# Kernel tuning notes

Hardware: AMD Instinct MI355X
Metric: run time of the kernel (lower is better)

## Reference

```python
import jax, jax.numpy as jnp
import numpy as np

H, D, BLK, R = 12, 64, 64, 3  # heads, size_per_head, block size, rand blocks
NEG = -1e9


def setup_inputs() -> dict:
    key = jax.random.key(0)
    ks = jax.random.split(key, 6)
    B, S, W = 2, 4096, H * D
    M = S // BLK
    return {
        "from_tensor": jax.random.normal(ks[0], (B, S, W), jnp.float32),
        "to_tensor": jax.random.normal(ks[1], (B, S, W), jnp.float32),
        "Wq": jax.random.normal(ks[2], (W, H * D), jnp.float32) * 0.02,
        "bq": jnp.zeros((H * D,), jnp.float32),
        "Wk": jax.random.normal(ks[3], (W, H * D), jnp.float32) * 0.02,
        "bk": jnp.zeros((H * D,), jnp.float32),
        "Wv": jax.random.normal(ks[4], (W, H * D), jnp.float32) * 0.02,
        "bv": jnp.zeros((H * D,), jnp.float32),
        "to_mask": jnp.ones((B, S), jnp.int32),
        "rand_attn": jax.random.randint(ks[5], (H, M - 2, R), 0, M - 2, jnp.int32),
    }


def _bigbird_block_sparse(from_tensor, to_tensor, Wq, bq, Wk, bk, Wv, bv, to_mask, rand_attn):
    B, S, _ = from_tensor.shape
    M = S // BLK
    scale = 1.0 / np.sqrt(D).astype(np.float32)

    # QKV projections -> [B,H,S,D]
    q = (from_tensor @ Wq + bq).reshape(B, S, H, D).transpose(0, 2, 1, 3)
    k = (to_tensor @ Wk + bk).reshape(B, S, H, D).transpose(0, 2, 1, 3)
    v = (to_tensor @ Wv + bv).reshape(B, S, H, D).transpose(0, 2, 1, 3)

    bq_ = q.reshape(B, H, M, BLK, D)
    bk_ = k.reshape(B, H, M, BLK, D)
    bv_ = v.reshape(B, H, M, BLK, D)

    tm = to_mask.astype(q.dtype)          # [B,S]
    bm = tm.reshape(B, M, BLK)            # [B,M,BLK]

    # gather random key/value blocks per head: [B,H,M-2,R*BLK,D]
    ha = jnp.arange(H)[:, None, None]
    gk = bk_[:, ha, rand_attn].reshape(B, H, M - 2, R * BLK, D)
    gv = bv_[:, ha, rand_attn].reshape(B, H, M - 2, R * BLK, D)
    gm = bm[:, rand_attn].reshape(B, H, M - 2, R * BLK)

    def full_row(qblk):  # first/last query blocks attend to everything
        s = jnp.einsum('bhqd,bhkd->bhqk', qblk, k) * scale + (1 - tm)[:, None, None, :] * NEG
        return jnp.einsum('bhqk,bhkd->bhqd', jax.nn.softmax(s, -1), v)

    def sparse_row(qblk, k_cat, v_cat, m_cat):  # [B,H,BLK,D] x [B,H,L,D]
        s = jnp.einsum('bhqd,bhkd->bhqk', qblk, k_cat) * scale + (1 - m_cat)[:, :, None, :] * NEG
        return jnp.einsum('bhqk,bhkd->bhqd', jax.nn.softmax(s, -1), v_cat)

    c_first = full_row(bq_[:, :, 0])
    c_last = full_row(bq_[:, :, M - 1])

    # second row: blocks [0,1,2,last] + rand
    k2 = jnp.concatenate([bk_[:, :, 0], bk_[:, :, 1], bk_[:, :, 2], bk_[:, :, M - 1], gk[:, :, 0]], axis=2)
    v2 = jnp.concatenate([bv_[:, :, 0], bv_[:, :, 1], bv_[:, :, 2], bv_[:, :, M - 1], gv[:, :, 0]], axis=2)
    m2s = jnp.concatenate([bm[:, 0], bm[:, 1], bm[:, 2], bm[:, M - 1]], axis=-1)
    m2 = jnp.concatenate([jnp.broadcast_to(m2s[:, None], (B, H, 4 * BLK)), gm[:, :, 0]], axis=-1)
    c_second = sparse_row(bq_[:, :, 1], k2, v2, m2)

    # second-to-last row: blocks [0,M-3,M-2,M-1] + rand
    k3 = jnp.concatenate([bk_[:, :, 0], bk_[:, :, M - 3], bk_[:, :, M - 2], bk_[:, :, M - 1], gk[:, :, M - 3]], axis=2)
    v3 = jnp.concatenate([bv_[:, :, 0], bv_[:, :, M - 3], bv_[:, :, M - 2], bv_[:, :, M - 1], gv[:, :, M - 3]], axis=2)
    m3s = jnp.concatenate([bm[:, 0], bm[:, M - 3], bm[:, M - 2], bm[:, M - 1]], axis=-1)
    m3 = jnp.concatenate([jnp.broadcast_to(m3s[:, None], (B, H, 4 * BLK)), gm[:, :, M - 3]], axis=-1)
    c_secondlast = sparse_row(bq_[:, :, M - 2], k3, v3, m3)

    # middle rows 2..M-3: band(prev,self,next) + rand + global first/last blocks
    L = M - 4
    band_k = jnp.concatenate([bk_[:, :, 1:M - 3], bk_[:, :, 2:M - 2], bk_[:, :, 3:M - 1]], axis=3)  # [B,H,L,3BLK,D]
    band_v = jnp.concatenate([bv_[:, :, 1:M - 3], bv_[:, :, 2:M - 2], bv_[:, :, 3:M - 1]], axis=3)
    band_m = jnp.concatenate([bm[:, 1:M - 3], bm[:, 2:M - 2], bm[:, 3:M - 1]], axis=-1)  # [B,L,3BLK]

    k_mid = jnp.concatenate([
        band_k, gk[:, :, 1:M - 3],
        jnp.broadcast_to(bk_[:, :, 0:1], (B, H, L, BLK, D)),
        jnp.broadcast_to(bk_[:, :, M - 1:M], (B, H, L, BLK, D))], axis=3)
    v_mid = jnp.concatenate([
        band_v, gv[:, :, 1:M - 3],
        jnp.broadcast_to(bv_[:, :, 0:1], (B, H, L, BLK, D)),
        jnp.broadcast_to(bv_[:, :, M - 1:M], (B, H, L, BLK, D))], axis=3)
    m_mid = jnp.concatenate([
        jnp.broadcast_to(band_m[:, None], (B, H, L, 3 * BLK)),
        gm[:, :, 1:M - 3],
        jnp.broadcast_to(bm[:, None, None, 0], (B, H, L, BLK)),
        jnp.broadcast_to(bm[:, None, None, M - 1], (B, H, L, BLK))], axis=-1)

    s_mid = jnp.einsum('bhlqd,bhlkd->bhlqk', bq_[:, :, 2:M - 2], k_mid) * scale
    s_mid = s_mid + (1 - m_mid)[:, :, :, None, :] * NEG
    c_mid = jnp.einsum('bhlqk,bhlkd->bhlqd', jax.nn.softmax(s_mid, -1), v_mid)

    ctx = jnp.concatenate([
        c_first[:, :, None], c_second[:, :, None], c_mid,
        c_secondlast[:, :, None], c_last[:, :, None]], axis=2)  # [B,H,M,BLK,D]
    return ctx.reshape(B, H, S, D).transpose(0, 2, 1, 3)  # [B,S,H,D]


def reference(from_tensor, to_tensor, Wq, bq, Wk, bk, Wv, bv, to_mask, rand_attn):
    return _bigbird_block_sparse(from_tensor, to_tensor, Wq, bq, Wk, bk, Wv, bv, to_mask, rand_attn)
```

## Files before the change

kernel.cpp:

```cpp
#include <hip/hip_runtime.h>

typedef __attribute__((ext_vector_type(4))) float f32x4;
typedef __attribute__((ext_vector_type(8))) __bf16 bf16x8;
typedef __attribute__((ext_vector_type(8))) unsigned short u16x8;
typedef __attribute__((ext_vector_type(4))) unsigned short u16x4;
typedef __attribute__((ext_vector_type(2))) unsigned int u32x2;

#define LOG2E 1.4426950408889634f

__device__ __forceinline__ unsigned short f2bf(float f) {
  unsigned u = __builtin_bit_cast(unsigned, f);
  u += 0x7fffu + ((u >> 16) & 1u);
  return (unsigned short)(u >> 16);
}

__device__ __forceinline__ unsigned cvtpk(float lo, float hi) {
  unsigned r;
  asm("v_cvt_pk_bf16_f32 %0, %1, %2" : "=v"(r) : "v"(lo), "v"(hi));
  return r;
}

__device__ __forceinline__ f32x4 mfma16(bf16x8 a, bf16x8 b, f32x4 c) {
  return __builtin_amdgcn_mfma_f32_16x16x32_bf16(a, b, c, 0, 0, 0);
}

__device__ __forceinline__ void gload_lds16(const void* g, void* l) {
  __builtin_amdgcn_global_load_lds(
      (const __attribute__((address_space(1))) void*)g,
      (__attribute__((address_space(3))) void*)l, 16, 0, 0);
}

#define NQK 6291456
#define NX 6291456
#define NW 589824

__global__ __launch_bounds__(256) void prep_kernel(
    const float* __restrict__ Wq, const float* __restrict__ Wk,
    const float* __restrict__ Wv, const float* __restrict__ from_t,
    const float* __restrict__ to_t, unsigned short* __restrict__ Wt,
    unsigned short* __restrict__ xb) {
  __shared__ float tile[64][65];
  const int bid = blockIdx.x;
  const int t = threadIdx.x;
  if (bid < 432) {
    const int z = bid / 144, rest = bid % 144;
    const float* __restrict__ src = (z == 0) ? Wq : (z == 1) ? Wk : Wv;
    unsigned short* __restrict__ dst = Wt + (size_t)z * NW;
    const int k0 = (rest / 12) * 64, n0 = (rest % 12) * 64;
    const int r = t >> 4, c4 = (t & 15) * 4;
#pragma unroll
    for (int p = 0; p < 4; ++p) {
      int rr = r + p * 16;
      f32x4 v = *(const f32x4*)(src + (size_t)(k0 + rr) * 768 + n0 + c4);
#pragma unroll
      for (int j = 0; j < 4; ++j) tile[rr][c4 + j] = v[j];
    }
    __syncthreads();
#pragma unroll
    for (int p = 0; p < 4; ++p) {
      int rn = r + p * 16;
      u16x4 o;
#pragma unroll
      for (int j = 0; j < 4; ++j) o[j] = f2bf(tile[c4 + j][rn]);
      *(u16x4*)(dst + (size_t)(n0 + rn) * 768 + k0 + c4) = o;
    }
  } else {
    const int idx = bid - 432;
    const int y = idx / 3072, xi = idx % 3072;
    const float* __restrict__ src = y ? to_t : from_t;
    unsigned short* __restrict__ dst = xb + (size_t)y * NX;
    const size_t i = ((size_t)xi * 256 + t) * 8;
    f32x4 a = *(const f32x4*)(src + i);
    f32x4 b = *(const f32x4*)(src + i + 4);
    u16x8 o;
#pragma unroll
    for (int j = 0; j < 4; ++j) { o[j] = f2bf(a[j]); o[j + 4] = f2bf(b[j]); }
    *(u16x8*)(dst + i) = o;
  }
}

__global__ __launch_bounds__(256) void qkv_gemm_kernel(
    const unsigned short* __restrict__ Xb, const unsigned short* __restrict__ Wt,
    const float* __restrict__ bq, const float* __restrict__ bk,
    const float* __restrict__ bv, unsigned short* __restrict__ qkvQK,
    unsigned short* __restrict__ vt, int zoff, int cpx) {
  __shared__ unsigned short A_lds[2][8192];
  __shared__ unsigned short B_lds[2][8192];
  const int bid0 = blockIdx.x;
  const int bid = (bid0 & 7) * cpx + (bid0 >> 3);
  const int z = zoff + bid / 384;
  const int rem = bid % 384;
  const int bm = rem / 6, bn = rem % 6;
  const unsigned short* __restrict__ X = Xb + (z ? (size_t)NX : 0);
  const unsigned short* __restrict__ Wz = Wt + (size_t)z * NW;
  const float* __restrict__ bias = (z == 0) ? bq : (z == 1) ? bk : bv;
  const int t = threadIdx.x, lane = t & 63, w = t >> 6;
  const int wm = (w >> 1) * 64, wn = (w & 1) * 64;
  const int l15 = lane & 15, cc = lane >> 4;

  f32x4 acc[4][4];
#pragma unroll
  for (int i = 0; i < 4; ++i)
#pragma unroll
    for (int j = 0; j < 4; ++j) acc[i][j] = (f32x4){0.f, 0.f, 0.f, 0.f};

  const unsigned short* Abase = X + (size_t)bm * 128 * 768;
  const unsigned short* Bbase = Wz + (size_t)bn * 128 * 768;

  auto STAGE = [&](int ks, int bufi) {
#pragma unroll
    for (int p = 0; p < 4; ++p) {
      int wb = p * 4 + w;
      int ch = wb * 64 + lane;
      int r = ch >> 3, sl = ch & 7;
      int g = sl ^ (r & 7);
      gload_lds16(Abase + (size_t)r * 768 + ks * 64 + g * 8,
                  &A_lds[bufi][wb * 512]);
      gload_lds16(Bbase + (size_t)r * 768 + ks * 64 + g * 8,
                  &B_lds[bufi][wb * 512]);
    }
  };

  STAGE(0, 0);
  __syncthreads();

  for (int ks = 0; ks < 12; ++ks) {
    const int cur = ks & 1;
    if (ks < 11) STAGE(ks + 1, cur ^ 1);

    bf16x8 af[4][2], bfr[4][2];
#pragma unroll
    for (int mi = 0; mi < 4; ++mi) {
      int row = wm + mi * 16 + l15;
      const char* rp = (const char*)A_lds[cur] + row * 128;
#pragma unroll
      for (int kk = 0; kk < 2; ++kk)
        af[mi][kk] = *(const bf16x8*)(rp + (((cc + 4 * kk) ^ (row & 7)) << 4));
    }
#pragma unroll
    for (int ni = 0; ni < 4; ++ni) {
      int row = wn + ni * 16 + l15;
      const char* rp = (const char*)B_lds[cur] + row * 128;
#pragma unroll
      for (int kk = 0; kk < 2; ++kk)
        bfr[ni][kk] = *(const bf16x8*)(rp + (((cc + 4 * kk) ^ (row & 7)) << 4));
    }
#pragma unroll
    for (int kk = 0; kk < 2; ++kk)
#pragma unroll
      for (int mi = 0; mi < 4; ++mi)
#pragma unroll
        for (int ni = 0; ni < 4; ++ni)
          acc[mi][ni] = mfma16(af[mi][kk], bfr[ni][kk], acc[mi][ni]);
    __syncthreads();
  }

  if (z < 2) {
    const float qscale = (z == 0) ? 0.125f * LOG2E : 1.0f;
    unsigned short* __restrict__ dst = qkvQK + (size_t)z * NQK;
#pragma unroll
    for (int ni = 0; ni < 4; ++ni) {
      int gn = bn * 128 + wn + ni * 16 + l15;
      float bv_ = bias[gn];
      int hh = gn >> 6, dd = gn & 63;
#pragma unroll
      for (int mi = 0; mi < 4; ++mi) {
#pragma unroll
        for (int r = 0; r < 4; ++r) {
          int gm = bm * 128 + wm + mi * 16 + cc * 4 + r;
          int bb = gm >> 12, s = gm & 4095;
          float val = (acc[mi][ni][r] + bv_) * qscale;
          dst[((((size_t)bb * 12 + hh) * 4096 + s) * 64) + dd] = f2bf(val);
        }
      }
    }
  } else {
#pragma unroll
    for (int ni = 0; ni < 4; ++ni) {
      int gn = bn * 128 + wn + ni * 16 + l15;
      float bv_ = bias[gn];
      int hh = gn >> 6, dd = gn & 63;
#pragma unroll
      for (int mi = 0; mi < 4; ++mi) {
        int gm0 = bm * 128 + wm + mi * 16 + cc * 4;
        int bb = gm0 >> 12, s0 = gm0 & 4095;
        u16x4 o;
#pragma unroll
        for (int r = 0; r < 4; ++r) o[r] = f2bf(acc[mi][ni][r] + bv_);
        *(u16x4*)(vt + ((size_t)(bb * 12 + hh) * 64 + dd) * 4096 + s0) = o;
      }
    }
  }
}

__global__ __launch_bounds__(256) void attn_kernel(
    const unsigned short* __restrict__ qkvQK, const unsigned short* __restrict__ vt,
    const int* __restrict__ to_mask, const int* __restrict__ rand_attn,
    float* __restrict__ out, float* __restrict__ part_o,
    float* __restrict__ part_ml) {
  __shared__ unsigned short K_lds[2][4096];
  __shared__ unsigned short VT_lds[2][4096];
  __shared__ unsigned short P_lds[4][1024];
  __shared__ float penal[8][64];
  __shared__ int blist[8];

  const int bid0 = blockIdx.x;
  const int bid = (bid0 & 7) * 234 + (bid0 >> 3);
  const int bh = bid / 78, r78 = bid % 78;
  const int h = bh % 12, b = bh / 12;
  const int t = threadIdx.x, lane = t & 63, w = t >> 6;
  const int l15 = lane & 15, cc = lane >> 4;

  int m, nblk, chunk = 0;
  bool full;
  if (r78 < 62) {
    full = false;
    m = r78 + 1;
    nblk = (m == 1 || m == 62) ? 7 : 8;
    if (t == 0) {
      const int* rp = rand_attn + ((size_t)h * 62 + (m - 1)) * 3;
      if (m == 1) {
        blist[0] = 0; blist[1] = 1; blist[2] = 2; blist[3] = 63;
        blist[4] = rp[0]; blist[5] = rp[1]; blist[6] = rp[2];
      } else if (m == 62) {
        blist[0] = 0; blist[1] = 61; blist[2] = 62; blist[3] = 63;
        blist[4] = rp[0]; blist[5] = rp[1]; blist[6] = rp[2];
      } else {
        blist[0] = m - 1; blist[1] = m; blist[2] = m + 1;
        blist[3] = rp[0]; blist[4] = rp[1]; blist[5] = rp[2];
        blist[6] = 0; blist[7] = 63;
      }
    }
  } else {
    full = true;
    int fr = r78 - 62;
    chunk = fr & 7;
    m = (fr >> 3) ? 63 : 0;
    nblk = 8;
    if (t < 8) blist[t] = chunk * 8 + t;
  }

  const unsigned short* qp = qkvQK + (((size_t)b * 12 + h) * 4096 + m * 64) * 64;
  const unsigned short* kp = qkvQK + NQK + (((size_t)b * 12 + h) * 4096) * 64;
  const unsigned short* vtp = vt + (((size_t)b * 12 + h) * 64) * 4096;

  int loff[2];
  const unsigned short *kpl[2], *vpl[2];
#pragma unroll
  for (int p = 0; p < 2; ++p) {
    int wb = p * 4 + w;
    int ch = wb * 64 + lane;
    int rr = ch >> 3;
    int g = (ch & 7) ^ (rr & 7);
    loff[p] = wb * 512;
    kpl[p] = kp + rr * 64 + g * 8;
    vpl[p] = vtp + rr * 4096 + g * 8;
  }

  bf16x8 aq[2];
  {
    int qrow = w * 16 + l15;
    aq[0] = *(const bf16x8*)(qp + qrow * 64 + cc * 8);
    aq[1] = *(const bf16x8*)(qp + qrow * 64 + 32 + cc * 8);
  }

  float m_run = -INFINITY, l_run = 0.f;
  f32x4 o_acc[4];
#pragma unroll
  for (int dg = 0; dg < 4; ++dg) o_acc[dg] = (f32x4){0.f, 0.f, 0.f, 0.f};

  char* pw = (char*)P_lds[w];
  const int swz = (l15 & 7) << 4;

  auto STAGE = [&](int kb, int bufi) {
    const size_t ko = (size_t)kb * 4096;
    const size_t vo = (size_t)kb * 64;
    gload_lds16(kpl[0] + ko, &K_lds[bufi][loff[0]]);
    gload_lds16(kpl[1] + ko, &K_lds[bufi][loff[1]]);
    gload_lds16(vpl[0] + vo, &VT_lds[bufi][loff[0]]);
    gload_lds16(vpl[1] + vo, &VT_lds[bufi][loff[1]]);
  };

  __syncthreads();

  {
    int ib = w;
#pragma unroll
    for (int pp = 0; pp < 2; ++pp, ib += 4)
      if (ib < nblk)
        penal[ib][lane] =
            (1.0f - (float)to_mask[(size_t)b * 4096 + blist[ib] * 64 + lane]) *
            (-1e9f * LOG2E);
  }
  STAGE(blist[0], 0);
  __syncthreads();

  for (int ib = 0; ib < nblk; ++ib) {
    const int cur = ib & 1;
    if (ib + 1 < nblk) STAGE(blist[ib + 1], cur ^ 1);

    float sm[4][4];
    const char* kbase = (const char*)K_lds[cur];
    __builtin_amdgcn_s_setprio(1);
#pragma unroll
    for (int kg = 0; kg < 4; ++kg) {
      int krow = kg * 16 + l15;
      const char* rp = kbase + krow * 128;
      int sz = (krow & 7) << 4;
      bf16x8 k0 = *(const bf16x8*)(rp + ((cc << 4) ^ sz));
      bf16x8 k1 = *(const bf16x8*)(rp + (((cc + 4) << 4) ^ sz));
      f32x4 zz = (f32x4){0.f, 0.f, 0.f, 0.f};
      zz = mfma16(k0, aq[0], zz);
      zz = mfma16(k1, aq[1], zz);
      f32x4 pen = *(const f32x4*)(&penal[ib][kg * 16 + cc * 4]);
#pragma unroll
      for (int r = 0; r < 4; ++r) sm[kg][r] = zz[r] + pen[r];
    }
    __builtin_amdgcn_s_setprio(0);

    float mk[4];
#pragma unroll
    for (int kg = 0; kg < 4; ++kg)
      mk[kg] = fmaxf(fmaxf(sm[kg][0], sm[kg][1]), fmaxf(sm[kg][2], sm[kg][3]));
    float mx = fmaxf(fmaxf(mk[0], mk[1]), fmaxf(mk[2], mk[3]));
    mx = fmaxf(mx, __shfl_xor(mx, 16, 64));
    mx = fmaxf(mx, __shfl_xor(mx, 32, 64));

    if (!__all(mx - m_run <= 8.0f)) {
      float mn = fmaxf(m_run, mx);
      float fac = exp2f(m_run - mn);
      m_run = mn;
      l_run *= fac;
      float fr_[4];
#pragma unroll
      for (int r = 0; r < 4; ++r) fr_[r] = __shfl(fac, cc * 4 + r, 64);
#pragma unroll
      for (int dg = 0; dg < 4; ++dg)
#pragma unroll
        for (int r = 0; r < 4; ++r) o_acc[dg][r] *= fr_[r];
    }

    float p_[4][4];
#pragma unroll
    for (int kg = 0; kg < 4; ++kg)
#pragma unroll
      for (int r = 0; r < 4; ++r) p_[kg][r] = exp2f(sm[kg][r] - m_run);
    float ss[4];
#pragma unroll
    for (int kg = 0; kg < 4; ++kg)
      ss[kg] = (p_[kg][0] + p_[kg][1]) + (p_[kg][2] + p_[kg][3]);
    float rs = (ss[0] + ss[1]) + (ss[2] + ss[3]);
    rs += __shfl_xor(rs, 16, 64);
    rs += __shfl_xor(rs, 32, 64);
    l_run += rs;

#pragma unroll
    for (int kg = 0; kg < 4; ++kg) {
      u32x2 wv;
      wv[0] = cvtpk(p_[kg][0], p_[kg][1]);
      wv[1] = cvtpk(p_[kg][2], p_[kg][3]);
      *(u32x2*)(pw + l15 * 128 + ((kg * 32 + cc * 8) ^ swz)) = wv;
    }
    __builtin_amdgcn_wave_barrier();
    bf16x8 ap0 = *(const bf16x8*)(pw + l15 * 128 + ((cc << 4) ^ swz));
    bf16x8 ap1 = *(const bf16x8*)(pw + l15 * 128 + (((cc + 4) << 4) ^ swz));

    const char* vbase = (const char*)VT_lds[cur];
    __builtin_amdgcn_s_setprio(1);
#pragma unroll
    for (int dg = 0; dg < 4; ++dg) {
      int drow = dg * 16 + l15;
      const char* vb = vbase + drow * 128;
      int sz = (drow & 7) << 4;
      bf16x8 v0 = *(const bf16x8*)(vb + ((cc << 4) ^ sz));
      bf16x8 v1 = *(const bf16x8*)(vb + (((cc + 4) << 4) ^ sz));
      o_acc[dg] = mfma16(ap0, v0, o_acc[dg]);
      o_acc[dg] = mfma16(ap1, v1, o_acc[dg]);
    }
    __builtin_amdgcn_s_setprio(0);
    __syncthreads();
  }

  if (!full) {
    float inv[4];
#pragma unroll
    for (int r = 0; r < 4; ++r) inv[r] = 1.0f / __shfl(l_run, cc * 4 + r, 64);
#pragma unroll
    for (int r = 0; r < 4; ++r) {
      int s = m * 64 + w * 16 + cc * 4 + r;
#pragma unroll
      for (int dg = 0; dg < 4; ++dg) {
        int d = dg * 16 + l15;
        out[(((size_t)b * 4096 + s) * 12 + h) * 64 + d] = o_acc[dg][r] * inv[r];
      }
    }
  } else {
    const int row = (b * 12 + h) * 2 + (m ? 1 : 0);
    float* po = part_o + (((size_t)row * 8 + chunk) * 64) * 64;
    float* pml = part_ml + ((size_t)row * 8 + chunk) * 128;
#pragma unroll
    for (int r = 0; r < 4; ++r) {
      int q = w * 16 + cc * 4 + r;
#pragma unroll
      for (int dg = 0; dg < 4; ++dg) {
        int d = dg * 16 + l15;
        po[q * 64 + d] = o_acc[dg][r];
      }
    }
    if (cc == 0) {
      pml[w * 16 + l15] = m_run;
      pml[64 + w * 16 + l15] = l_run;
    }
  }
}

__global__ __launch_bounds__(256) void combine_kernel(
    const float* __restrict__ part_o, const float* __restrict__ part_ml,
    float* __restrict__ out) {
  const int row = blockIdx.x;
  const int b = row / 24, h = (row >> 1) % 12, m = (row & 1) ? 63 : 0;
  const int t = threadIdx.x;
  const int q = t >> 2, d0 = (t & 3) * 16;

  float mc[8], lc[8];
  float M = -INFINITY;
#pragma unroll
  for (int c = 0; c < 8; ++c) {
    const float* pml = part_ml + ((size_t)row * 8 + c) * 128;
    mc[c] = pml[q];
    lc[c] = pml[64 + q];
    M = fmaxf(M, mc[c]);
  }
  float wgt[8], L = 0.f;
#pragma unroll
  for (int c = 0; c < 8; ++c) {
    wgt[c] = exp2f(mc[c] - M);
    L += wgt[c] * lc[c];
  }
  f32x4 acc[4];
#pragma unroll
  for (int j = 0; j < 4; ++j) acc[j] = (f32x4){0.f, 0.f, 0.f, 0.f};
#pragma unroll
  for (int c = 0; c < 8; ++c) {
    const float* po = part_o + (((size_t)row * 8 + c) * 64 + q) * 64 + d0;
#pragma unroll
    for (int j = 0; j < 4; ++j) {
      f32x4 v = *(const f32x4*)(po + j * 4);
#pragma unroll
      for (int e = 0; e < 4; ++e) acc[j][e] += wgt[c] * v[e];
    }
  }
  const float inv = 1.0f / L;
  const int s = m * 64 + q;
  float* op = out + (((size_t)b * 4096 + s) * 12 + h) * 64 + d0;
#pragma unroll
  for (int j = 0; j < 4; ++j) {
    f32x4 v;
#pragma unroll
    for (int e = 0; e < 4; ++e) v[e] = acc[j][e] * inv;
    *(f32x4*)(op + j * 4) = v;
  }
}

extern "C" void kernel_launch(void* const* d_in, const int* in_sizes, int n_in,
                              void* d_out, int out_size, void* d_ws,
                              size_t ws_size, hipStream_t stream) {
  (void)in_sizes; (void)n_in; (void)out_size;
  const float* from_t = (const float*)d_in[0];
  const float* to_t = (const float*)d_in[1];
  const float* Wq = (const float*)d_in[2];
  const float* bq = (const float*)d_in[3];
  const float* Wk = (const float*)d_in[4];
  const float* bk = (const float*)d_in[5];
  const float* Wv = (const float*)d_in[6];
  const float* bv = (const float*)d_in[7];
  const int* to_mask = (const int*)d_in[8];
  const int* rand_attn = (const int*)d_in[9];
  float* out = (float*)d_out;

  unsigned short* Wt = (unsigned short*)d_ws;
  unsigned short* qkvQK = Wt + (size_t)3 * NW;
  unsigned short* Xb = qkvQK + (size_t)2 * NQK;

  const size_t part_elems = (size_t)48 * 8 * 64 * 64 + (size_t)48 * 8 * 128;
  const size_t fused_bytes =
      ((size_t)3 * NW + 2 * NQK + 2 * NX + NQK) * 2 + part_elems * 4;

  if (ws_size >= fused_bytes) {
    unsigned short* vt = Xb + (size_t)2 * NX;
    float* part_o = (float*)Xb;
    float* part_ml = part_o + (size_t)48 * 8 * 64 * 64;

    prep_kernel<<<dim3(6576), dim3(256), 0, stream>>>(Wq, Wk, Wv, from_t, to_t,
                                                      Wt, Xb);
    qkv_gemm_kernel<<<dim3(1152), dim3(256), 0, stream>>>(
        Xb, Wt, bq, bk, bv, qkvQK, vt, 0, 144);
    attn_kernel<<<dim3(1872), dim3(256), 0, stream>>>(
        qkvQK, vt, to_mask, rand_attn, out, part_o, part_ml);
    combine_kernel<<<dim3(48), dim3(256), 0, stream>>>(part_o, part_ml, out);
  } else {
    unsigned short* vt = Xb;
    float* part_o = (float*)(Xb + (size_t)NX);
    float* part_ml = part_o + (size_t)48 * 8 * 64 * 64;

    prep_kernel<<<dim3(6576), dim3(256), 0, stream>>>(Wq, Wk, Wv, from_t, to_t,
                                                      Wt, Xb);
    qkv_gemm_kernel<<<dim3(768), dim3(256), 0, stream>>>(
        Xb, Wt, bq, bk, bv, qkvQK, vt, 0, 96);
    qkv_gemm_kernel<<<dim3(384), dim3(256), 0, stream>>>(
        Xb, Wt, bq, bk, bv, qkvQK, vt, 2, 48);
    attn_kernel<<<dim3(1872), dim3(256), 0, stream>>>(
        qkvQK, vt, to_mask, rand_attn, out, part_o, part_ml);
    combine_kernel<<<dim3(48), dim3(256), 0, stream>>>(part_o, part_ml, out);
  }
}
```

Before: 115.1 us.

## Halve QKV GEMM k-tile, load V fragments directly from global in attention

The QKV GEMM now stages 32-wide k slices instead of 64, which halves its LDS footprint and doubles the number of loop iterations and barriers. The attention kernel drops the V^T LDS staging and loads V fragments straight from global memory into registers at the start of each block iteration. It also fuses the exp/sum/pack softmax loops and sets launch bounds to 4 blocks per SM. The goal is higher occupancy from less LDS use. The cost is exposed global-load latency for V and extra synchronisation in the GEMM.

After: 159.9 us. +39.0%, slower.

```diff
diff --git a/kernel.cpp b/kernel.cpp
--- a/kernel.cpp
+++ b/kernel.cpp
@@ -84,8 +84,8 @@
     const float* __restrict__ bq, const float* __restrict__ bk,
     const float* __restrict__ bv, unsigned short* __restrict__ qkvQK,
     unsigned short* __restrict__ vt, int zoff, int cpx) {
-  __shared__ unsigned short A_lds[2][8192];
-  __shared__ unsigned short B_lds[2][8192];
+  __shared__ unsigned short A_lds[2][4096];
+  __shared__ unsigned short B_lds[2][4096];
   const int bid0 = blockIdx.x;
   const int bid = (bid0 & 7) * cpx + (bid0 >> 3);
   const int z = zoff + bid / 384;
@@ -109,14 +109,14 @@
 
   auto STAGE = [&](int ks, int bufi) {
 #pragma unroll
-    for (int p = 0; p < 4; ++p) {
+    for (int p = 0; p < 2; ++p) {
       int wb = p * 4 + w;
       int ch = wb * 64 + lane;
-      int r = ch >> 3, sl = ch & 7;
-      int g = sl ^ (r & 7);
-      gload_lds16(Abase + (size_t)r * 768 + ks * 64 + g * 8,
+      int r = ch >> 2, sl = ch & 3;
+      int g = sl ^ (r & 3);
+      gload_lds16(Abase + (size_t)r * 768 + ks * 32 + g * 8,
                   &A_lds[bufi][wb * 512]);
-      gload_lds16(Bbase + (size_t)r * 768 + ks * 64 + g * 8,
+      gload_lds16(Bbase + (size_t)r * 768 + ks * 32 + g * 8,
                   &B_lds[bufi][wb * 512]);
     }
   };
@@ -124,34 +124,28 @@
   STAGE(0, 0);
   __syncthreads();
 
-  for (int ks = 0; ks < 12; ++ks) {
+  for (int ks = 0; ks < 24; ++ks) {
     const int cur = ks & 1;
-    if (ks < 11) STAGE(ks + 1, cur ^ 1);
-
-    bf16x8 af[4][2], bfr[4][2];
+    if (ks < 23) STAGE(ks + 1, cur ^ 1);
+
+    bf16x8 af[4], bfr[4];
 #pragma unroll
     for (int mi = 0; mi < 4; ++mi) {
       int row = wm + mi * 16 + l15;
-      const char* rp = (const char*)A_lds[cur] + row * 128;
-#pragma unroll
-      for (int kk = 0; kk < 2; ++kk)
-        af[mi][kk] = *(const bf16x8*)(rp + (((cc + 4 * kk) ^ (row & 7)) << 4));
+      af[mi] = *(const bf16x8*)((const char*)A_lds[cur] + row * 64 +
+                                ((cc ^ (row & 3)) << 4));
     }
 #pragma unroll
     for (int ni = 0; ni < 4; ++ni) {
       int row = wn + ni * 16 + l15;
-      const char* rp = (const char*)B_lds[cur] + row * 128;
-#pragma unroll
-      for (int kk = 0; kk < 2; ++kk)
-        bfr[ni][kk] = *(const bf16x8*)(rp + (((cc + 4 * kk) ^ (row & 7)) << 4));
-    }
-#pragma unroll
-    for (int kk = 0; kk < 2; ++kk)
-#pragma unroll
-      for (int mi = 0; mi < 4; ++mi)
-#pragma unroll
-        for (int ni = 0; ni < 4; ++ni)
-          acc[mi][ni] = mfma16(af[mi][kk], bfr[ni][kk], acc[mi][ni]);
+      bfr[ni] = *(const bf16x8*)((const char*)B_lds[cur] + row * 64 +
+                                 ((cc ^ (row & 3)) << 4));
+    }
+#pragma unroll
+    for (int mi = 0; mi < 4; ++mi)
+#pragma unroll
+      for (int ni = 0; ni < 4; ++ni)
+        acc[mi][ni] = mfma16(af[mi], bfr[ni], acc[mi][ni]);
     __syncthreads();
   }
 
@@ -193,13 +187,12 @@
   }
 }
 
-__global__ __launch_bounds__(256) void attn_kernel(
+__global__ __launch_bounds__(256, 4) void attn_kernel(
     const unsigned short* __restrict__ qkvQK, const unsigned short* __restrict__ vt,
     const int* __restrict__ to_mask, const int* __restrict__ rand_attn,
     float* __restrict__ out, float* __restrict__ part_o,
     float* __restrict__ part_ml) {
   __shared__ unsigned short K_lds[2][4096];
-  __shared__ unsigned short VT_lds[2][4096];
   __shared__ unsigned short P_lds[4][1024];
   __shared__ float penal[8][64];
   __shared__ int blist[8];
@@ -245,7 +238,7 @@
   const unsigned short* vtp = vt + (((size_t)b * 12 + h) * 64) * 4096;
 
   int loff[2];
-  const unsigned short *kpl[2], *vpl[2];
+  const unsigned short* kpl[2];
 #pragma unroll
   for (int p = 0; p < 2; ++p) {
     int wb = p * 4 + w;
@@ -254,8 +247,8 @@
     int g = (ch & 7) ^ (rr & 7);
     loff[p] = wb * 512;
     kpl[p] = kp + rr * 64 + g * 8;
-    vpl[p] = vtp + rr * 4096 + g * 8;
-  }
+  }
+  const unsigned short* vbase_ = vtp + (size_t)l15 * 4096 + cc * 8;
 
   bf16x8 aq[2];
   {
@@ -274,11 +267,8 @@
 
   auto STAGE = [&](int kb, int bufi) {
     const size_t ko = (size_t)kb * 4096;
-    const size_t vo = (size_t)kb * 64;
     gload_lds16(kpl[0] + ko, &K_lds[bufi][loff[0]]);
     gload_lds16(kpl[1] + ko, &K_lds[bufi][loff[1]]);
-    gload_lds16(vpl[0] + vo, &VT_lds[bufi][loff[0]]);
-    gload_lds16(vpl[1] + vo, &VT_lds[bufi][loff[1]]);
   };
 
   __syncthreads();
@@ -297,7 +287,16 @@
 
   for (int ib = 0; ib < nblk; ++ib) {
     const int cur = ib & 1;
+    const int kb = blist[ib];
     if (ib + 1 < nblk) STAGE(blist[ib + 1], cur ^ 1);
+
+    bf16x8 vf0[4], vf1[4];
+#pragma unroll
+    for (int dg = 0; dg < 4; ++dg) {
+      const unsigned short* cp = vbase_ + (size_t)dg * 16 * 4096 + kb * 64;
+      vf0[dg] = *(const bf16x8*)(cp);
+      vf1[dg] = *(const bf16x8*)(cp + 32);
+    }
 
     float sm[4][4];
     const char* kbase = (const char*)K_lds[cur];
@@ -340,42 +339,30 @@
         for (int r = 0; r < 4; ++r) o_acc[dg][r] *= fr_[r];
     }
 
-    float p_[4][4];
-#pragma unroll
-    for (int kg = 0; kg < 4; ++kg)
-#pragma unroll
-      for (int r = 0; r < 4; ++r) p_[kg][r] = exp2f(sm[kg][r] - m_run);
-    float ss[4];
-#pragma unroll
-    for (int kg = 0; kg < 4; ++kg)
-      ss[kg] = (p_[kg][0] + p_[kg][1]) + (p_[kg][2] + p_[kg][3]);
-    float rs = (ss[0] + ss[1]) + (ss[2] + ss[3]);
+    float rs = 0.f;
+#pragma unroll
+    for (int kg = 0; kg < 4; ++kg) {
+      float p0 = exp2f(sm[kg][0] - m_run), p1 = exp2f(sm[kg][1] - m_run);
+      float p2 = exp2f(sm[kg][2] - m_run), p3 = exp2f(sm[kg][3] - m_run);
+      rs += (p0 + p1) + (p2 + p3);
+      u32x2 wv;
+      wv[0] = cvtpk(p0, p1);
+      wv[1] = cvtpk(p2, p3);
+      *(u32x2*)(pw + l15 * 128 + ((kg * 32 + cc * 8) ^ swz)) = wv;
+    }
     rs += __shfl_xor(rs, 16, 64);
     rs += __shfl_xor(rs, 32, 64);
     l_run += rs;
 
-#pragma unroll
-    for (int kg = 0; kg < 4; ++kg) {
-      u32x2 wv;
-      wv[0] = cvtpk(p_[kg][0], p_[kg][1]);
-      wv[1] = cvtpk(p_[kg][2], p_[kg][3]);
-      *(u32x2*)(pw + l15 * 128 + ((kg * 32 + cc * 8) ^ swz)) = wv;
-    }
     __builtin_amdgcn_wave_barrier();
     bf16x8 ap0 = *(const bf16x8*)(pw + l15 * 128 + ((cc << 4) ^ swz));
     bf16x8 ap1 = *(const bf16x8*)(pw + l15 * 128 + (((cc + 4) << 4) ^ swz));
 
-    const char* vbase = (const char*)VT_lds[cur];
     __builtin_amdgcn_s_setprio(1);
 #pragma unroll
     for (int dg = 0; dg < 4; ++dg) {
-      int drow = dg * 16 + l15;
-      const char* vb = vbase + drow * 128;
-      int sz = (drow & 7) << 4;
-      bf16x8 v0 = *(const bf16x8*)(vb + ((cc << 4) ^ sz));
-      bf16x8 v1 = *(const bf16x8*)(vb + (((cc + 4) << 4) ^ sz));
-      o_acc[dg] = mfma16(ap0, v0, o_acc[dg]);
-      o_acc[dg] = mfma16(ap1, v1, o_acc[dg]);
+      o_acc[dg] = mfma16(ap0, vf0[dg], o_acc[dg]);
+      o_acc[dg] = mfma16(ap1, vf1[dg], o_acc[dg]);
     }
     __builtin_amdgcn_s_setprio(0);
     __syncthreads();
```

## Deepen attention K/V prefetch to triple-stage ring and use fine-grained vmcnt waits

Applied to the files above, without the earlier changes.

The attention kernel grows its K/V LDS ring from 2 to 4 buffers and prefetches two blocks ahead. It replaces the full __syncthreads at the end of each iteration with explicit vmcnt waits and a single barrier at the top. The QKV GEMM gets the same treatment with partial vmcnt waits, so the next stage's global-to-LDS loads can stay in flight while compute proceeds. Other changes drop the s_setprio hints and fuse the exp/sum/pack loops. The cost is twice the LDS use in attention, which may lower occupancy, and correctness now depends on hand-counted vmcnt values matching the number of issued loads.

Measured after the change: 116.7 us. About the same (+1.4%).

```diff
diff --git a/kernel.cpp b/kernel.cpp
--- a/kernel.cpp
+++ b/kernel.cpp
@@ -122,11 +122,17 @@
   };
 
   STAGE(0, 0);
-  __syncthreads();
 
   for (int ks = 0; ks < 12; ++ks) {
     const int cur = ks & 1;
-    if (ks < 11) STAGE(ks + 1, cur ^ 1);
+    if (ks < 11) {
+      STAGE(ks + 1, cur ^ 1);
+      asm volatile("s_waitcnt vmcnt(8)" ::: "memory");
+    } else {
+      asm volatile("s_waitcnt vmcnt(0)" ::: "memory");
+    }
+    __builtin_amdgcn_s_barrier();
+    __builtin_amdgcn_sched_barrier(0);
 
     bf16x8 af[4][2], bfr[4][2];
 #pragma unroll
@@ -152,7 +158,8 @@
 #pragma unroll
         for (int ni = 0; ni < 4; ++ni)
           acc[mi][ni] = mfma16(af[mi][kk], bfr[ni][kk], acc[mi][ni]);
-    __syncthreads();
+    asm volatile("s_waitcnt lgkmcnt(0)" ::: "memory");
+    __builtin_amdgcn_s_barrier();
   }
 
   if (z < 2) {
@@ -198,8 +205,8 @@
     const int* __restrict__ to_mask, const int* __restrict__ rand_attn,
     float* __restrict__ out, float* __restrict__ part_o,
     float* __restrict__ part_ml) {
-  __shared__ unsigned short K_lds[2][4096];
-  __shared__ unsigned short VT_lds[2][4096];
+  __shared__ unsigned short K_lds[4][4096];
+  __shared__ unsigned short VT_lds[4][4096];
   __shared__ unsigned short P_lds[4][1024];
   __shared__ float penal[8][64];
   __shared__ int blist[8];
@@ -293,15 +300,25 @@
             (-1e9f * LOG2E);
   }
   STAGE(blist[0], 0);
-  __syncthreads();
+  STAGE(blist[1], 1);
+  asm volatile("s_waitcnt lgkmcnt(0)" ::: "memory");
+  __builtin_amdgcn_s_barrier();
 
   for (int ib = 0; ib < nblk; ++ib) {
-    const int cur = ib & 1;
-    if (ib + 1 < nblk) STAGE(blist[ib + 1], cur ^ 1);
+    const int bi = ib & 3;
+    if (ib + 2 < nblk) {
+      STAGE(blist[ib + 2], (ib + 2) & 3);
+      asm volatile("s_waitcnt vmcnt(8)" ::: "memory");
+    } else if (ib + 1 < nblk) {
+      asm volatile("s_waitcnt vmcnt(4)" ::: "memory");
+    } else {
+      asm volatile("s_waitcnt vmcnt(0)" ::: "memory");
+    }
+    __builtin_amdgcn_s_barrier();
+    __builtin_amdgcn_sched_barrier(0);
 
     float sm[4][4];
-    const char* kbase = (const char*)K_lds[cur];
-    __builtin_amdgcn_s_setprio(1);
+    const char* kbase = (const char*)K_lds[bi];
 #pragma unroll
     for (int kg = 0; kg < 4; ++kg) {
       int krow = kg * 16 + l15;
@@ -316,7 +333,6 @@
 #pragma unroll
       for (int r = 0; r < 4; ++r) sm[kg][r] = zz[r] + pen[r];
     }
-    __builtin_amdgcn_s_setprio(0);
 
     float mk[4];
 #pragma unroll
@@ -340,33 +356,26 @@
         for (int r = 0; r < 4; ++r) o_acc[dg][r] *= fr_[r];
     }
 
-    float p_[4][4];
-#pragma unroll
-    for (int kg = 0; kg < 4; ++kg)
-#pragma unroll
-      for (int r = 0; r < 4; ++r) p_[kg][r] = exp2f(sm[kg][r] - m_run);
-    float ss[4];
-#pragma unroll
-    for (int kg = 0; kg < 4; ++kg)
-      ss[kg] = (p_[kg][0] + p_[kg][1]) + (p_[kg][2] + p_[kg][3]);
-    float rs = (ss[0] + ss[1]) + (ss[2] + ss[3]);
+    float rs = 0.f;
+#pragma unroll
+    for (int kg = 0; kg < 4; ++kg) {
+      float p0 = exp2f(sm[kg][0] - m_run), p1 = exp2f(sm[kg][1] - m_run);
+      float p2 = exp2f(sm[kg][2] - m_run), p3 = exp2f(sm[kg][3] - m_run);
+      rs += (p0 + p1) + (p2 + p3);
+      u32x2 wv;
+      wv[0] = cvtpk(p0, p1);
+      wv[1] = cvtpk(p2, p3);
+      *(u32x2*)(pw + l15 * 128 + ((kg * 32 + cc * 8) ^ swz)) = wv;
+    }
     rs += __shfl_xor(rs, 16, 64);
     rs += __shfl_xor(rs, 32, 64);
     l_run += rs;
 
-#pragma unroll
-    for (int kg = 0; kg < 4; ++kg) {
-      u32x2 wv;
-      wv[0] = cvtpk(p_[kg][0], p_[kg][1]);
-      wv[1] = cvtpk(p_[kg][2], p_[kg][3]);
-      *(u32x2*)(pw + l15 * 128 + ((kg * 32 + cc * 8) ^ swz)) = wv;
-    }
     __builtin_amdgcn_wave_barrier();
     bf16x8 ap0 = *(const bf16x8*)(pw + l15 * 128 + ((cc << 4) ^ swz));
     bf16x8 ap1 = *(const bf16x8*)(pw + l15 * 128 + (((cc + 4) << 4) ^ swz));
 
-    const char* vbase = (const char*)VT_lds[cur];
-    __builtin_amdgcn_s_setprio(1);
+    const char* vbase = (const char*)VT_lds[bi];
 #pragma unroll
     for (int dg = 0; dg < 4; ++dg) {
       int drow = dg * 16 + l15;
@@ -377,8 +386,6 @@
       o_acc[dg] = mfma16(ap0, v0, o_acc[dg]);
       o_acc[dg] = mfma16(ap1, v1, o_acc[dg]);
     }
-    __builtin_amdgcn_s_setprio(0);
-    __syncthreads();
   }
 
   if (!full) {
```
